# Optimization experiments

Hardware: AMD Instinct MI355X
Metric: run time of the kernel (lower is better)

Reference implementation:

```python
import jax, jax.numpy as jnp
import numpy as np


def conv3d(x, w, b):
    # x: [B,C,T,H,W], w: [O,I,3,3,3], padding=1, stride=1
    y = jax.lax.conv_general_dilated(
        x, w, window_strides=(1, 1, 1), padding=((1, 1), (1, 1), (1, 1)),
        dimension_numbers=('NCDHW', 'OIDHW', 'NCDHW'))
    return y + b[None, :, None, None, None]


def deform_conv3d(x, offsets, w, b):
    # Deformable 3D conv, kernel 3, pad 1, stride 1, no modulation mask.
    # offsets: [B, 81, T, H, W] -> [B, 27, 3(t,h,w), T, H, W]
    B, Cin, T, H, W = x.shape
    nk = 27
    off = offsets.reshape(B, nk, 3, T, H, W)
    r = jnp.arange(3, dtype=x.dtype) - 1.0  # kernel taps {-1,0,1}
    kt, kh, kw = jnp.meshgrid(r, r, r, indexing='ij')
    koff = jnp.stack([kt.ravel(), kh.ravel(), kw.ravel()], axis=-1)  # [27,3]
    bt = jnp.arange(T, dtype=x.dtype)[:, None, None]
    bh = jnp.arange(H, dtype=x.dtype)[None, :, None]
    bw = jnp.arange(W, dtype=x.dtype)[None, None, :]
    base = jnp.stack(jnp.broadcast_arrays(bt, bh, bw), axis=0)  # [3,T,H,W]
    pos = base[None, None] + koff[None, :, :, None, None, None] + off  # [B,27,3,T,H,W]
    pt, ph, pw = pos[:, :, 0], pos[:, :, 1], pos[:, :, 2]
    ft, fh, fw = jnp.floor(pt), jnp.floor(ph), jnp.floor(pw)
    at, ah, aw = pt - ft, ph - fh, pw - fw
    it, ih, iw = ft.astype(jnp.int32), fh.astype(jnp.int32), fw.astype(jnp.int32)
    N = T * H * W
    xf = x.reshape(B, Cin, N)
    gather = jax.vmap(lambda xb, lb: xb[:, lb])  # ([Cin,N],[27,N])->[Cin,27,N]
    acc = jnp.zeros((B, Cin, nk, N), dtype=x.dtype)
    # trilinear interpolation: accumulate 8 corners, zero outside bounds
    for dt in (0, 1):
        tti = it + dt
        wt = (1.0 - at) if dt == 0 else at
        vt = (tti >= 0) & (tti < T)
        tc = jnp.clip(tti, 0, T - 1)
        for dh in (0, 1):
            hhi = ih + dh
            wh = (1.0 - ah) if dh == 0 else ah
            vh = (hhi >= 0) & (hhi < H)
            hc = jnp.clip(hhi, 0, H - 1)
            for dw in (0, 1):
                wwi = iw + dw
                ww = (1.0 - aw) if dw == 0 else aw
                vw = (wwi >= 0) & (wwi < W)
                wc = jnp.clip(wwi, 0, W - 1)
                wgt = (wt * wh * ww) * (vt & vh & vw).astype(x.dtype)  # [B,27,T,H,W]
                lin = (tc * H + hc) * W + wc  # [B,27,T,H,W]
                g = gather(xf, lin.reshape(B, nk, N))  # [B,Cin,27,N]
                acc = acc + wgt.reshape(B, 1, nk, N) * g
    out = jnp.einsum('oik,bikn->bon', w.reshape(w.shape[0], Cin, nk), acc)
    out = out + b[None, :, None]
    return out.reshape(B, w.shape[0], T, H, W)


def setup_inputs() -> dict:
    key = jax.random.key(0)
    ks = jax.random.split(key, 12)
    B, Cin, Cout, mdim = 1, 256, 256, 256
    T, H, W = 8, 24, 24

    def winit(k, shape):
        fan_in = int(np.prod(shape[1:]))
        return jax.random.normal(k, shape, jnp.float32) / np.float32(np.sqrt(fan_in))

    return {
        'x': jax.random.normal(ks[0], (B, Cin, T, H, W), jnp.float32),
        'l1_w': winit(ks[1], (mdim, Cin, 3, 3, 3)),
        'l1_b': jnp.zeros((mdim,), jnp.float32),
        'l2_w': winit(ks[2], (mdim, mdim, 3, 3, 3)),
        'l2_b': jnp.zeros((mdim,), jnp.float32),
        'l3_w': winit(ks[3], (mdim, mdim, 3, 3, 3)),
        'l3_b': jnp.zeros((mdim,), jnp.float32),
        'def_w': winit(ks[4], (81, mdim, 3, 3, 3)) * 0.1,  # keep offsets small
        'def_b': jnp.zeros((81,), jnp.float32),
        'c3d_w': winit(ks[5], (Cout, Cin, 3, 3, 3)),
        'c3d_b': jnp.zeros((Cout,), jnp.float32),
    }


def reference(x, l1_w, l1_b, l2_w, l2_b, l3_w, l3_b, def_w, def_b, c3d_w, c3d_b):
    h = jax.nn.relu(conv3d(x, l1_w, l1_b))
    h = jax.nn.relu(conv3d(h, l2_w, l2_b))
    h = jax.nn.relu(conv3d(h, l3_w, l3_b))
    offsets = conv3d(h, def_w, def_b)  # [B,81,T,H,W]
    return deform_conv3d(x, offsets, c3d_w, c3d_b)
```

## Files before the change

### kernel.cpp

```cpp
#include <hip/hip_runtime.h>

#define TT 8
#define HH 24
#define WW 24
#define NN 4608
#define CIN 256
#define N3 6760
#define KDIM 6912
#define BK 64
#define KTILES 108
#define NSPLIT 9
#define KT_PER 12

typedef short short8 __attribute__((ext_vector_type(8)));
typedef short short4v __attribute__((ext_vector_type(4)));
typedef float f32x4  __attribute__((ext_vector_type(4)));
typedef int   i32x4  __attribute__((ext_vector_type(4)));
typedef unsigned int u32x4 __attribute__((ext_vector_type(4)));

#define MFMA16 __builtin_amdgcn_mfma_f32_16x16x32_bf16

__device__ __forceinline__ short f2bf(float f) {
    unsigned u = __float_as_uint(f);
    unsigned r = u + 0x7fffu + ((u >> 16) & 1u);
    return (short)(r >> 16);
}
__device__ __forceinline__ float bf2f(short s) {
    return __uint_as_float(((unsigned)(unsigned short)s) << 16);
}

__device__ __forceinline__ int n3_of(int n) {
    int t = n / (HH * WW), r = n % (HH * WW), h = r / WW, w = r % WW;
    return ((t + 1) * 26 + (h + 1)) * 26 + (w + 1);
}

__device__ __forceinline__ void gload16(const void* gsrc, void* lds) {
    __builtin_amdgcn_global_load_lds(
        (const __attribute__((address_space(1))) void*)gsrc,
        (__attribute__((address_space(3))) void*)lds, 16, 0, 0);
}

__global__ __launch_bounds__(256) void transpose_k(const float* __restrict__ x,
                                                   short* __restrict__ xbf3) {
    __shared__ float T[64][65];
    const int lane = threadIdx.x & 63, wave = threadIdx.x >> 6;
    const int n0 = blockIdx.x * 64, ci0 = blockIdx.y * 64;
    #pragma unroll
    for (int j = 0; j < 16; ++j) {
        int ci_l = wave * 16 + j;
        T[ci_l][lane] = x[(size_t)(ci0 + ci_l) * NN + n0 + lane];
    }
    __syncthreads();
    #pragma unroll
    for (int j = 0; j < 16; ++j) {
        int n_l = wave * 16 + j;
        xbf3[(size_t)n3_of(n0 + n_l) * 256 + ci0 + lane] = f2bf(T[lane][n_l]);
    }
}

__global__ __launch_bounds__(256) void repack_all_k(
    const float* __restrict__ w1, const float* __restrict__ w2,
    const float* __restrict__ w3, const float* __restrict__ wc,
    const float* __restrict__ wd,
    short* __restrict__ d1, short* __restrict__ d2,
    short* __restrict__ d3, short* __restrict__ dc,
    short* __restrict__ dd) {
    __shared__ float buf[KDIM];
    const int sel = blockIdx.y, o = blockIdx.x, ci = threadIdx.x;
    const float* w; short* dst; int Cout = 256;
    if      (sel == 0) { w = w1; dst = d1; }
    else if (sel == 1) { w = w2; dst = d2; }
    else if (sel == 2) { w = w3; dst = d3; }
    else if (sel == 3) { w = wc; dst = dc; }
    else               { w = wd; dst = dd; Cout = 81; if (o >= 128) return; }

    if (o < Cout) {
        const float* src = w + (size_t)o * KDIM;
        #pragma unroll
        for (int j = 0; j < 27; ++j)
            buf[j * 256 + ci] = src[j * 256 + ci];
    }
    __syncthreads();

    const int row = o & 127, y = o >> 7;
    #pragma unroll
    for (int k = 0; k < 27; ++k) {
        int K = k * 256 + ci;
        int kt = K >> 6, kk = K & 63;
        int slot = (kk >> 3) ^ (row & 7), e = kk & 7;
        size_t idx = ((size_t)(y * KTILES + kt)) * 8192 + row * 64 + slot * 8 + e;
        float v = (o < Cout) ? buf[ci * 27 + k] : 0.f;
        dst[idx] = f2bf(v);
    }
}

__global__ __launch_bounds__(256) void sample_k(
    const short* __restrict__ xbf3, const float* __restrict__ offs,
    short* __restrict__ S)
{
    __shared__ char recs[64 * 64];
    const int k = blockIdx.y, n0 = blockIdx.x * 64;
    const int tid = threadIdx.x;

    if (tid < 64) {
        const int n = n0 + tid;
        const int t = n / (HH * WW), r = n % (HH * WW), h = r / WW, w2 = r % WW;
        const int ki = k / 9, kj = (k % 9) / 3, kl = k % 3;
        const float pt = (float)(t  + ki - 1) + offs[(size_t)(k * 3 + 0) * NN + n];
        const float ph = (float)(h  + kj - 1) + offs[(size_t)(k * 3 + 1) * NN + n];
        const float pw = (float)(w2 + kl - 1) + offs[(size_t)(k * 3 + 2) * NN + n];
        const float ft = floorf(pt), fh = floorf(ph), fw = floorf(pw);
        const float at = pt - ft, ah = ph - fh, aw = pw - fw;
        const int it = (int)ft, ih = (int)fh, iw = (int)fw;
        i32x4 idx[2]; f32x4 wgt[2];
        #pragma unroll
        for (int dt = 0; dt < 2; ++dt)
        #pragma unroll
        for (int dh = 0; dh < 2; ++dh)
        #pragma unroll
        for (int dw = 0; dw < 2; ++dw) {
            const int c = (dt * 2 + dh) * 2 + dw;
            const int ti = it + dt, hi = ih + dh, wi = iw + dw;
            const bool v = (ti >= 0) && (ti < TT) && (hi >= 0) && (hi < HH) && (wi >= 0) && (wi < WW);
            float wv = (dt ? at : 1.f - at) * (dh ? ah : 1.f - ah) * (dw ? aw : 1.f - aw);
            const int tc = min(max(ti, 0), TT - 1), hc = min(max(hi, 0), HH - 1), wc = min(max(wi, 0), WW - 1);
            const int r3 = ((tc + 1) * 26 + (hc + 1)) * 26 + (wc + 1);
            idx[c >> 2][c & 3] = r3 * 512;
            wgt[c >> 2][c & 3] = v ? wv : 0.f;
        }
        char* rec = &recs[tid * 64];
        *(i32x4*)(rec)      = idx[0];
        *(i32x4*)(rec + 16) = idx[1];
        *(f32x4*)(rec + 32) = wgt[0];
        *(f32x4*)(rec + 48) = wgt[1];
    }
    __syncthreads();

    const int lane = tid & 63, wave = tid >> 6;
    const int half = lane >> 5, lch = lane & 31;
    const char* xb = (const char*)xbf3 + lch * 16;
    short* Sk = S + (size_t)k * NN * 256 + lch * 8;

    for (int i = 0; i < 16; i += 4) {
        const int na = wave * 16 + i + half;
        const int nb = na + 2;
        const char* ra = &recs[na * 64];
        const char* rb = &recs[nb * 64];
        const i32x4 ia0 = *(const i32x4*)(ra);
        const i32x4 ia1 = *(const i32x4*)(ra + 16);
        const f32x4 wa0 = *(const f32x4*)(ra + 32);
        const f32x4 wa1 = *(const f32x4*)(ra + 48);
        const i32x4 ib0 = *(const i32x4*)(rb);
        const i32x4 ib1 = *(const i32x4*)(rb + 16);
        const f32x4 wb0 = *(const f32x4*)(rb + 32);
        const f32x4 wb1 = *(const f32x4*)(rb + 48);

        u32x4 ga[8], gb[8];
        #pragma unroll
        for (int c = 0; c < 4; ++c) {
            ga[c]     = *(const u32x4*)(xb + ia0[c]);
            ga[c + 4] = *(const u32x4*)(xb + ia1[c]);
            gb[c]     = *(const u32x4*)(xb + ib0[c]);
            gb[c + 4] = *(const u32x4*)(xb + ib1[c]);
        }

        float sa[8] = {}, sb[8] = {};
        #pragma unroll
        for (int c = 0; c < 8; ++c) {
            const float va = (c < 4) ? wa0[c & 3] : wa1[c & 3];
            const float vb = (c < 4) ? wb0[c & 3] : wb1[c & 3];
            #pragma unroll
            for (int j = 0; j < 4; ++j) {
                sa[2*j]   = fmaf(va, __uint_as_float(ga[c][j] << 16),         sa[2*j]);
                sa[2*j+1] = fmaf(va, __uint_as_float(ga[c][j] & 0xffff0000u), sa[2*j+1]);
                sb[2*j]   = fmaf(vb, __uint_as_float(gb[c][j] << 16),         sb[2*j]);
                sb[2*j+1] = fmaf(vb, __uint_as_float(gb[c][j] & 0xffff0000u), sb[2*j+1]);
            }
        }
        short8 oa, ob;
        #pragma unroll
        for (int m = 0; m < 8; ++m) { oa[m] = f2bf(sa[m]); ob[m] = f2bf(sb[m]); }
        *(short8*)(Sk + (size_t)(n0 + na) * 256) = oa;
        *(short8*)(Sk + (size_t)(n0 + nb) * 256) = ob;
    }
}

template<int CP>
__global__ __launch_bounds__(256, 3) void gemm_conv_sk(
    const short* __restrict__ src,
    const short* __restrict__ wrb_sw,
    short* __restrict__ P)
{
    __shared__ short Ap[8192];
    __shared__ short Bw[8192];
    const int tid = threadIdx.x;
    const int l = tid & 63, w = tid >> 6;
    const int n0 = blockIdx.x * 128, co0 = blockIdx.y * 128, split = blockIdx.z;
    const int wr = w >> 1, wc = w & 1;
    const int lm = l & 15, lq = l >> 4;
    const int rswz = (lm & 7) << 3;
    const int kt0 = split * KT_PER;

    const int colA = 8 * ((l & 7) ^ ((l >> 3) & 7));
    int r3[4];
    #pragma unroll
    for (int j = 0; j < 4; ++j)
        r3[j] = n3_of(n0 + w * 32 + j * 8 + (l >> 3));
    const short* bbase = wrb_sw + ((size_t)blockIdx.y * KTILES) * 8192 + (w * 4) * 512 + l * 8;

    f32x4 acc[4][4] = {};

    for (int i = 0; i < KT_PER; ++i) {
        const int kt = kt0 + i;
        const int k = kt >> 2, ci0 = (kt & 3) * 64;
        const int dt = k / 9 - 1, dh = (k % 9) / 3 - 1, dw = k % 3 - 1;
        const int d3 = (dt * 26 + dh) * 26 + dw;
        #pragma unroll
        for (int j = 0; j < 4; ++j)
            gload16(src + (size_t)(r3[j] + d3) * 256 + ci0 + colA, &Ap[(w * 4 + j) * 512]);
        const short* b = bbase + (size_t)kt * 8192;
        #pragma unroll
        for (int j = 0; j < 4; ++j)
            gload16(b + j * 512, &Bw[(w * 4 + j) * 512]);
        __syncthreads();
        #pragma unroll
        for (int ks = 0; ks < 2; ++ks) {
            const int c = (ks * 32 + lq * 8) ^ rswz;
            short8 a[4], bf[4];
            #pragma unroll
            for (int m = 0; m < 4; ++m)
                a[m] = *(const short8*)&Ap[(wr * 64 + m * 16 + lm) * 64 + c];
            #pragma unroll
            for (int nb = 0; nb < 4; ++nb)
                bf[nb] = *(const short8*)&Bw[(wc * 64 + nb * 16 + lm) * 64 + c];
            #pragma unroll
            for (int m = 0; m < 4; ++m)
            #pragma unroll
            for (int nb = 0; nb < 4; ++nb)
                acc[m][nb] = MFMA16(a[m], bf[nb], acc[m][nb], 0, 0, 0);
        }
        __syncthreads();
    }
    #pragma unroll
    for (int m = 0; m < 4; ++m)
    #pragma unroll
    for (int nb = 0; nb < 4; ++nb) {
        int co = co0 + wc * 64 + nb * 16 + lm;
        int n = n0 + wr * 64 + m * 16 + lq * 4;
        short4v o;
        #pragma unroll
        for (int j = 0; j < 4; ++j) o[j] = f2bf(acc[m][nb][j]);
        *(short4v*)(P + ((size_t)split * CP + co) * NN + n) = o;
    }
}

__global__ __launch_bounds__(256, 3) void gemm_deform_sk(
    const short* __restrict__ S,
    const short* __restrict__ wrb_sw,
    short* __restrict__ P)
{
    __shared__ short Ap[8192];
    __shared__ short Bw[8192];
    const int tid = threadIdx.x;
    const int l = tid & 63, w = tid >> 6;
    const int n0 = blockIdx.x * 128, co0 = blockIdx.y * 128, split = blockIdx.z;
    const int wr = w >> 1, wc = w & 1;
    const int lm = l & 15, lq = l >> 4;
    const int rswz = (lm & 7) << 3;
    const int kt0 = split * KT_PER;

    const int colA = 8 * ((l & 7) ^ ((l >> 3) & 7));
    int rA[4];
    #pragma unroll
    for (int j = 0; j < 4; ++j)
        rA[j] = n0 + w * 32 + j * 8 + (l >> 3);
    const short* bbase = wrb_sw + ((size_t)blockIdx.y * KTILES) * 8192 + (w * 4) * 512 + l * 8;

    f32x4 acc[4][4] = {};

    for (int i = 0; i < KT_PER; ++i) {
        const int kt = kt0 + i;
        const int k = kt >> 2, ci0 = (kt & 3) * 64;
        #pragma unroll
        for (int j = 0; j < 4; ++j)
            gload16(S + ((size_t)k * NN + rA[j]) * 256 + ci0 + colA, &Ap[(w * 4 + j) * 512]);
        const short* b = bbase + (size_t)kt * 8192;
        #pragma unroll
        for (int j = 0; j < 4; ++j)
            gload16(b + j * 512, &Bw[(w * 4 + j) * 512]);
        __syncthreads();
        #pragma unroll
        for (int ks = 0; ks < 2; ++ks) {
            const int c = (ks * 32 + lq * 8) ^ rswz;
            short8 a[4], bf[4];
            #pragma unroll
            for (int m = 0; m < 4; ++m)
                a[m] = *(const short8*)&Ap[(wr * 64 + m * 16 + lm) * 64 + c];
            #pragma unroll
            for (int nb = 0; nb < 4; ++nb)
                bf[nb] = *(const short8*)&Bw[(wc * 64 + nb * 16 + lm) * 64 + c];
            #pragma unroll
            for (int m = 0; m < 4; ++m)
            #pragma unroll
            for (int nb = 0; nb < 4; ++nb)
                acc[m][nb] = MFMA16(a[m], bf[nb], acc[m][nb], 0, 0, 0);
        }
        __syncthreads();
    }
    #pragma unroll
    for (int m = 0; m < 4; ++m)
    #pragma unroll
    for (int nb = 0; nb < 4; ++nb) {
        int co = co0 + wc * 64 + nb * 16 + lm;
        int n = n0 + wr * 64 + m * 16 + lq * 4;
        short4v o;
        #pragma unroll
        for (int j = 0; j < 4; ++j) o[j] = f2bf(acc[m][nb][j]);
        *(short4v*)(P + ((size_t)split * 256 + co) * NN + n) = o;
    }
}

template<bool RELU>
__global__ __launch_bounds__(256) void reduce_k(
    const short* __restrict__ P, const float* __restrict__ bias,
    float* __restrict__ dst, int Cout, int CP)
{
    int id = blockIdx.x * 256 + threadIdx.x;
    int total = Cout * (NN / 4);
    if (id >= total) return;
    int co = id / (NN / 4), n4 = id - co * (NN / 4);
    const short* p0 = P + ((size_t)co) * NN + n4 * 4;
    float v[4] = {};
    #pragma unroll
    for (int s = 0; s < NSPLIT; ++s) {
        short4v u = *(const short4v*)(p0 + (size_t)s * CP * NN);
        #pragma unroll
        for (int q = 0; q < 4; ++q) v[q] += bf2f(u[q]);
    }
    float bv = bias[co];
    f32x4 o;
    #pragma unroll
    for (int q = 0; q < 4; ++q) {
        float f = v[q] + bv;
        if (RELU) f = fmaxf(f, 0.f);
        o[q] = f;
    }
    *(f32x4*)(dst + (size_t)co * NN + n4 * 4) = o;
}

__global__ __launch_bounds__(256) void reduce_bf3(
    const short* __restrict__ P, const float* __restrict__ bias,
    short* __restrict__ dst)
{
    __shared__ float T[64][65];
    const int lane = threadIdx.x & 63, wave = threadIdx.x >> 6;
    const int n0 = blockIdx.x * 64, co0 = blockIdx.y * 64;
    #pragma unroll
    for (int j = 0; j < 16; ++j) {
        int co_l = wave * 16 + j, co = co0 + co_l;
        const short* p0 = P + (size_t)co * NN + n0 + lane;
        float a = 0.f;
        #pragma unroll
        for (int s = 0; s < NSPLIT; ++s) a += bf2f(p0[(size_t)s * 256 * NN]);
        T[co_l][lane] = fmaxf(a + bias[co], 0.f);
    }
    __syncthreads();
    #pragma unroll
    for (int j = 0; j < 16; ++j) {
        int n_l = wave * 16 + j;
        dst[(size_t)n3_of(n0 + n_l) * 256 + co0 + lane] = f2bf(T[lane][n_l]);
    }
}

extern "C" void kernel_launch(void* const* d_in, const int* in_sizes, int n_in,
                              void* d_out, int out_size, void* d_ws, size_t ws_size,
                              hipStream_t stream)
{
    const float* x   = (const float*)d_in[0];
    const float* l1w = (const float*)d_in[1];
    const float* l1b = (const float*)d_in[2];
    const float* l2w = (const float*)d_in[3];
    const float* l2b = (const float*)d_in[4];
    const float* l3w = (const float*)d_in[5];
    const float* l3b = (const float*)d_in[6];
    const float* dfw = (const float*)d_in[7];
    const float* dfb = (const float*)d_in[8];
    const float* c3w = (const float*)d_in[9];
    const float* c3b = (const float*)d_in[10];
    float* out = (float*)d_out;

    char* base = (char*)d_ws;
    short* S    = (short*)base;
    short* h1b  = (short*)(base);
    short* h2b  = (short*)(base + 3461120);
    short* h3b  = (short*)(base + 6922240);
    short* wrb1 = (short*)(base + 10383360);
    short* wrb2 = (short*)(base + 13922304);
    short* wrb3 = (short*)(base + 17461248);
    short* wrbd = (short*)(base + 21000192);
    char* q = base + 63700992;
    short* xbf3 = (short*)q; q += 3461120;
    float* offs = (float*)q; q += 1492992;
    short* wrbc = (short*)q; q += 3538944;
    short* P    = (short*)q;

    hipMemsetAsync(xbf3, 0, (size_t)N3 * 256 * 2, stream);
    hipMemsetAsync(h1b,  0, (size_t)3 * N3 * 256 * 2, stream);

    transpose_k<<<dim3(72, 4), dim3(256), 0, stream>>>(x, xbf3);
    repack_all_k<<<dim3(256, 5), dim3(256), 0, stream>>>(l1w, l2w, l3w, c3w, dfw,
                                                         wrb1, wrb2, wrb3, wrbc, wrbd);

    const dim3 blk(256);
    const int rg81 = (81 * (NN / 4) + 255) / 256;
    const int rg256 = (256 * (NN / 4) + 255) / 256;

    gemm_conv_sk<256><<<dim3(36, 2, NSPLIT), blk, 0, stream>>>(xbf3, wrb1, P);
    reduce_bf3       <<<dim3(72, 4),         blk, 0, stream>>>(P, l1b, h1b);
    gemm_conv_sk<256><<<dim3(36, 2, NSPLIT), blk, 0, stream>>>(h1b, wrb2, P);
    reduce_bf3       <<<dim3(72, 4),         blk, 0, stream>>>(P, l2b, h2b);
    gemm_conv_sk<256><<<dim3(36, 2, NSPLIT), blk, 0, stream>>>(h2b, wrb3, P);
    reduce_bf3       <<<dim3(72, 4),         blk, 0, stream>>>(P, l3b, h3b);
    gemm_conv_sk<128><<<dim3(36, 1, NSPLIT), blk, 0, stream>>>(h3b, wrbd, P);
    reduce_k<false>  <<<dim3(rg81),          blk, 0, stream>>>(P, dfb, offs, 81, 128);

    sample_k<<<dim3(72, 27), blk, 0, stream>>>(xbf3, offs, S);
    gemm_deform_sk<<<dim3(36, 2, NSPLIT), blk, 0, stream>>>(S, wrbc, P);
    reduce_k<false><<<dim3(rg256), blk, 0, stream>>>(P, c3b, out, 256, 256);
}
```

Baseline: 205.6 us.

## Fuse prep kernels and memsets, fold offset split-K reduction into sampler

Merges the input transpose, weight repacking and halo zeroing into a single prep kernel, replacing two full-buffer memsets with writes to border rows only. The separate reduce kernel for the offset conv is dropped: the sampling kernel now sums the split-K partials and adds the bias directly when it computes sample positions. This removes several launches and a round trip through an fp32 offsets buffer. In exchange the sampler does extra loads per point, and the halo zeroing is serialized within few blocks.

```diff
diff --git a/kernel.cpp b/kernel.cpp
--- a/kernel.cpp
+++ b/kernel.cpp
@@ -40,63 +40,79 @@
         (__attribute__((address_space(3))) void*)lds, 16, 0, 0);
 }
 
-__global__ __launch_bounds__(256) void transpose_k(const float* __restrict__ x,
-                                                   short* __restrict__ xbf3) {
-    __shared__ float T[64][65];
-    const int lane = threadIdx.x & 63, wave = threadIdx.x >> 6;
-    const int n0 = blockIdx.x * 64, ci0 = blockIdx.y * 64;
-    #pragma unroll
-    for (int j = 0; j < 16; ++j) {
-        int ci_l = wave * 16 + j;
-        T[ci_l][lane] = x[(size_t)(ci0 + ci_l) * NN + n0 + lane];
-    }
-    __syncthreads();
-    #pragma unroll
-    for (int j = 0; j < 16; ++j) {
-        int n_l = wave * 16 + j;
-        xbf3[(size_t)n3_of(n0 + n_l) * 256 + ci0 + lane] = f2bf(T[lane][n_l]);
-    }
-}
-
-__global__ __launch_bounds__(256) void repack_all_k(
+__global__ __launch_bounds__(256) void prep_k(
+    const float* __restrict__ x,
     const float* __restrict__ w1, const float* __restrict__ w2,
     const float* __restrict__ w3, const float* __restrict__ wc,
     const float* __restrict__ wd,
     short* __restrict__ d1, short* __restrict__ d2,
-    short* __restrict__ d3, short* __restrict__ dc,
-    short* __restrict__ dd) {
-    __shared__ float buf[KDIM];
-    const int sel = blockIdx.y, o = blockIdx.x, ci = threadIdx.x;
-    const float* w; short* dst; int Cout = 256;
-    if      (sel == 0) { w = w1; dst = d1; }
-    else if (sel == 1) { w = w2; dst = d2; }
-    else if (sel == 2) { w = w3; dst = d3; }
-    else if (sel == 3) { w = wc; dst = dc; }
-    else               { w = wd; dst = dd; Cout = 81; if (o >= 128) return; }
-
-    if (o < Cout) {
-        const float* src = w + (size_t)o * KDIM;
-        #pragma unroll
-        for (int j = 0; j < 27; ++j)
-            buf[j * 256 + ci] = src[j * 256 + ci];
-    }
-    __syncthreads();
-
-    const int row = o & 127, y = o >> 7;
-    #pragma unroll
-    for (int k = 0; k < 27; ++k) {
-        int K = k * 256 + ci;
-        int kt = K >> 6, kk = K & 63;
-        int slot = (kk >> 3) ^ (row & 7), e = kk & 7;
-        size_t idx = ((size_t)(y * KTILES + kt)) * 8192 + row * 64 + slot * 8 + e;
-        float v = (o < Cout) ? buf[ci * 27 + k] : 0.f;
-        dst[idx] = f2bf(v);
+    short* __restrict__ d3, short* __restrict__ dc, short* __restrict__ dd,
+    short* __restrict__ xbf3, short* __restrict__ h1b)
+{
+    __shared__ char smem[27648];
+    const int sel = blockIdx.y;
+
+    if (sel < 5) {
+        if (blockIdx.x >= 256) return;
+        const int o = blockIdx.x, ci = threadIdx.x;
+        const float* w; short* dst; int Cout = 256;
+        if      (sel == 0) { w = w1; dst = d1; }
+        else if (sel == 1) { w = w2; dst = d2; }
+        else if (sel == 2) { w = w3; dst = d3; }
+        else if (sel == 3) { w = wc; dst = dc; }
+        else               { w = wd; dst = dd; Cout = 81; if (o >= 128) return; }
+        float* buf = (float*)smem;
+        if (o < Cout) {
+            const float* src = w + (size_t)o * KDIM;
+            #pragma unroll
+            for (int j = 0; j < 27; ++j)
+                buf[j * 256 + ci] = src[j * 256 + ci];
+        }
+        __syncthreads();
+        const int row = o & 127, y = o >> 7;
+        #pragma unroll
+        for (int k = 0; k < 27; ++k) {
+            int K = k * 256 + ci;
+            int kt = K >> 6, kk = K & 63;
+            int slot = (kk >> 3) ^ (row & 7), e = kk & 7;
+            size_t idx = ((size_t)(y * KTILES + kt)) * 8192 + row * 64 + slot * 8 + e;
+            float v = (o < Cout) ? buf[ci * 27 + k] : 0.f;
+            dst[idx] = f2bf(v);
+        }
+    } else if (sel == 5) {
+        float (*T)[65] = (float(*)[65])smem;
+        const int bx = blockIdx.x;
+        const int n0 = (bx % 72) * 64, ci0 = (bx / 72) * 64;
+        const int lane = threadIdx.x & 63, wave = threadIdx.x >> 6;
+        #pragma unroll
+        for (int j = 0; j < 16; ++j) {
+            int ci_l = wave * 16 + j;
+            T[ci_l][lane] = x[(size_t)(ci0 + ci_l) * NN + n0 + lane];
+        }
+        __syncthreads();
+        #pragma unroll
+        for (int j = 0; j < 16; ++j) {
+            int n_l = wave * 16 + j;
+            xbf3[(size_t)n3_of(n0 + n_l) * 256 + ci0 + lane] = f2bf(T[lane][n_l]);
+        }
+    } else {
+        const int tid = threadIdx.x;
+        for (int r = blockIdx.x * 27; r < min((int)(blockIdx.x * 27 + 27), N3); ++r) {
+            int t3 = r / 676, rem = r % 676, h3 = rem / 26, w3 = rem % 26;
+            bool interior = (t3 >= 1 && t3 <= 8 && h3 >= 1 && h3 <= 24 && w3 >= 1 && w3 <= 24);
+            if (!interior && tid < 128) {
+                ((unsigned*)(xbf3 + (size_t)r * 256))[tid] = 0;
+                ((unsigned*)(h1b  + (size_t)r * 256))[tid] = 0;
+                ((unsigned*)(h1b + 1730560 + (size_t)r * 256))[tid] = 0;
+                ((unsigned*)(h1b + 3461120 + (size_t)r * 256))[tid] = 0;
+            }
+        }
     }
 }
 
 __global__ __launch_bounds__(256) void sample_k(
-    const short* __restrict__ xbf3, const float* __restrict__ offs,
-    short* __restrict__ S)
+    const short* __restrict__ xbf3, const short* __restrict__ Poff,
+    const float* __restrict__ dfb, short* __restrict__ S)
 {
     __shared__ char recs[64 * 64];
     const int k = blockIdx.y, n0 = blockIdx.x * 64;
@@ -106,9 +122,19 @@
         const int n = n0 + tid;
         const int t = n / (HH * WW), r = n % (HH * WW), h = r / WW, w2 = r % WW;
         const int ki = k / 9, kj = (k % 9) / 3, kl = k % 3;
-        const float pt = (float)(t  + ki - 1) + offs[(size_t)(k * 3 + 0) * NN + n];
-        const float ph = (float)(h  + kj - 1) + offs[(size_t)(k * 3 + 1) * NN + n];
-        const float pw = (float)(w2 + kl - 1) + offs[(size_t)(k * 3 + 2) * NN + n];
+        float po[3];
+        #pragma unroll
+        for (int d = 0; d < 3; ++d) {
+            const int ch = k * 3 + d;
+            float a = 0.f;
+            #pragma unroll
+            for (int s = 0; s < NSPLIT; ++s)
+                a += bf2f(Poff[((size_t)(s * 128 + ch)) * NN + n]);
+            po[d] = a + dfb[ch];
+        }
+        const float pt = (float)(t  + ki - 1) + po[0];
+        const float ph = (float)(h  + kj - 1) + po[1];
+        const float pw = (float)(w2 + kl - 1) + po[2];
         const float ft = floorf(pt), fh = floorf(ph), fw = floorf(pw);
         const float at = pt - ft, ah = ph - fh, aw = pw - fw;
         const int it = (int)ft, ih = (int)fh, iw = (int)fw;
@@ -392,27 +418,22 @@
     char* base = (char*)d_ws;
     short* S    = (short*)base;
     short* h1b  = (short*)(base);
-    short* h2b  = (short*)(base + 3461120);
-    short* h3b  = (short*)(base + 6922240);
     short* wrb1 = (short*)(base + 10383360);
     short* wrb2 = (short*)(base + 13922304);
     short* wrb3 = (short*)(base + 17461248);
     short* wrbd = (short*)(base + 21000192);
+    short* h2b  = (short*)(base + 3461120);
+    short* h3b  = (short*)(base + 6922240);
     char* q = base + 63700992;
     short* xbf3 = (short*)q; q += 3461120;
-    float* offs = (float*)q; q += 1492992;
     short* wrbc = (short*)q; q += 3538944;
     short* P    = (short*)q;
 
-    hipMemsetAsync(xbf3, 0, (size_t)N3 * 256 * 2, stream);
-    hipMemsetAsync(h1b,  0, (size_t)3 * N3 * 256 * 2, stream);
-
-    transpose_k<<<dim3(72, 4), dim3(256), 0, stream>>>(x, xbf3);
-    repack_all_k<<<dim3(256, 5), dim3(256), 0, stream>>>(l1w, l2w, l3w, c3w, dfw,
-                                                         wrb1, wrb2, wrb3, wrbc, wrbd);
-
     const dim3 blk(256);
-    const int rg81 = (81 * (NN / 4) + 255) / 256;
+    prep_k<<<dim3(288, 7), blk, 0, stream>>>(x, l1w, l2w, l3w, c3w, dfw,
+                                             wrb1, wrb2, wrb3, wrbc, wrbd,
+                                             xbf3, h1b);
+
     const int rg256 = (256 * (NN / 4) + 255) / 256;
 
     gemm_conv_sk<256><<<dim3(36, 2, NSPLIT), blk, 0, stream>>>(xbf3, wrb1, P);
@@ -422,9 +443,8 @@
     gemm_conv_sk<256><<<dim3(36, 2, NSPLIT), blk, 0, stream>>>(h2b, wrb3, P);
     reduce_bf3       <<<dim3(72, 4),         blk, 0, stream>>>(P, l3b, h3b);
     gemm_conv_sk<128><<<dim3(36, 1, NSPLIT), blk, 0, stream>>>(h3b, wrbd, P);
-    reduce_k<false>  <<<dim3(rg81),          blk, 0, stream>>>(P, dfb, offs, 81, 128);
-
-    sample_k<<<dim3(72, 27), blk, 0, stream>>>(xbf3, offs, S);
+
+    sample_k<<<dim3(72, 27), blk, 0, stream>>>(xbf3, P, dfb, S);
     gemm_deform_sk<<<dim3(36, 2, NSPLIT), blk, 0, stream>>>(S, wrbc, P);
     reduce_k<false><<<dim3(rg256), blk, 0, stream>>>(P, c3b, out, 256, 256);
 }
```

New measurement: 195.6 us (median of 3 runs). 1.05x faster.
